# Performance work log

Measured on AMD Instinct MI355X. Metric: run time of the kernel, lower is better.

Reference implementation:

```python
import jax, jax.numpy as jnp
import numpy as np

D_MODEL = 2048
NUM_HEADS = 32
NUM_KV_GROUPS = 8
D_K = D_MODEL // NUM_HEADS  # 64
KV_DIM = D_K * NUM_KV_GROUPS  # 512
B, S = 2, 2048


def setup_inputs() -> dict:
    key = jax.random.key(0)
    ks = jax.random.split(key, 9)
    sd = 1.0 / np.sqrt(D_MODEL).astype(np.float32)
    return {
        "x": jax.random.normal(ks[0], (B, S, D_MODEL), jnp.float32),
        "wq": jax.random.normal(ks[1], (D_MODEL, D_MODEL), jnp.float32) * sd,
        "bq": jnp.zeros((D_MODEL,), jnp.float32),
        "wk": jax.random.normal(ks[2], (D_MODEL, KV_DIM), jnp.float32) * sd,
        "bk": jnp.zeros((KV_DIM,), jnp.float32),
        "wv": jax.random.normal(ks[3], (D_MODEL, KV_DIM), jnp.float32) * sd,
        "bv": jnp.zeros((KV_DIM,), jnp.float32),
        "wo": jax.random.normal(ks[4], (D_MODEL, D_MODEL), jnp.float32) * sd,
        "bo": jnp.zeros((D_MODEL,), jnp.float32),
    }


def reference(x, wq, bq, wk, bk, wv, bv, wo, bo):
    b, s, _ = x.shape
    # projections (torch Linear = x @ W^T + b; weights here stored as (in,out))
    Q = (x @ wq + bq).reshape(b, s, NUM_HEADS, D_K).transpose(0, 2, 1, 3)       # [B,H,S,dk]
    K = (x @ wk + bk).reshape(b, s, NUM_KV_GROUPS, D_K).transpose(0, 2, 1, 3)   # [B,G,S,dk]
    V = (x @ wv + bv).reshape(b, s, NUM_KV_GROUPS, D_K).transpose(0, 2, 1, 3)   # [B,G,S,dk]
    kv_repeat = NUM_HEADS // NUM_KV_GROUPS
    K_rep = jnp.repeat(K, kv_repeat, axis=1)  # [B,H,S,dk]
    V_rep = jnp.repeat(V, kv_repeat, axis=1)  # [B,H,S,dk]
    scale = 1.0 / jnp.sqrt(jnp.asarray(D_K, x.dtype))
    attn_scores = jnp.einsum("bhqd,bhkd->bhqk", Q, K_rep) * scale
    attn_weights = jax.nn.softmax(attn_scores, axis=-1)                          # [B,H,S,S]
    context = jnp.einsum("bhqk,bhkd->bhqd", attn_weights, V_rep)
    context = context.transpose(0, 2, 1, 3).reshape(b, s, D_MODEL)
    return context @ wo + bo
```

## Files before the change

kernel.cpp:

```cpp
#include <hip/hip_runtime.h>
#include <hip/hip_bf16.h>

typedef __bf16 v8bf16 __attribute__((ext_vector_type(8)));
typedef __bf16 bf16x4 __attribute__((ext_vector_type(4)));
typedef float  f32x4  __attribute__((ext_vector_type(4)));

#define D_MODEL 2048
#define S_LEN   2048
#define NHEADS  32
#define NGROUPS 8
#define DK      64
#define NTOK    4096
#define NQKV    3072
#define QSCALE  0.18033688011112042f

__device__ __forceinline__ void lds_load16(const void* g, void* l) {
  __builtin_amdgcn_global_load_lds(
      (__attribute__((address_space(1))) unsigned int*)g,
      (__attribute__((address_space(3))) unsigned int*)l, 16, 0, 0);
}

__global__ __launch_bounds__(256)
void cvt_f32_bf16(const float* __restrict__ in, __bf16* __restrict__ out, int n) {
  int i = (blockIdx.x * 256 + threadIdx.x) * 4;
  if (i >= n) return;
  float4 v = *(const float4*)(in + i);
  bf16x4 o = { (__bf16)v.x, (__bf16)v.y, (__bf16)v.z, (__bf16)v.w };
  *(bf16x4*)(out + i) = o;
}

__global__ __launch_bounds__(256)
void transpose_cvt(const float* __restrict__ in, __bf16* __restrict__ out, int R, int C) {
  __shared__ float tile[32][33];
  int tx = threadIdx.x, ty = threadIdx.y;
  int c0 = blockIdx.x * 32, r0 = blockIdx.y * 32;
#pragma unroll
  for (int j = 0; j < 4; j++)
    tile[ty + 8 * j][tx] = in[(size_t)(r0 + ty + 8 * j) * C + c0 + tx];
  __syncthreads();
#pragma unroll
  for (int j = 0; j < 4; j++)
    out[(size_t)(c0 + ty + 8 * j) * R + r0 + tx] = (__bf16)tile[tx][ty + 8 * j];
}

__global__ __launch_bounds__(256)
void transpose_bf16(const __bf16* __restrict__ in, __bf16* __restrict__ out,
                    int R, int C, int ldin, int ldout) {
  __shared__ __bf16 tile[32][33];
  int tx = threadIdx.x, ty = threadIdx.y;
  int c0 = blockIdx.x * 32, r0 = blockIdx.y * 32;
#pragma unroll
  for (int j = 0; j < 4; j++)
    tile[ty + 8 * j][tx] = in[(size_t)(r0 + ty + 8 * j) * ldin + c0 + tx];
  __syncthreads();
#pragma unroll
  for (int j = 0; j < 4; j++)
    out[(size_t)(c0 + ty + 8 * j) * ldout + r0 + tx] = tile[tx][ty + 8 * j];
}

template <int MODE>
__global__ __launch_bounds__(256, 2)
void gemm_bt(const __bf16* __restrict__ A, const __bf16* __restrict__ BT,
             const float* __restrict__ b0, const float* __restrict__ b1,
             const float* __restrict__ b2,
             __bf16* __restrict__ Cb, float* __restrict__ Cf,
             int M, int N, int K) {
  __shared__ __bf16 As[128 * 32];
  __shared__ __bf16 Bs[128 * 32];
  const int t = threadIdx.x;
  const int lane = t & 63, w = t >> 6;
  const int lr = lane & 15, lg = lane >> 4;
  const int gx = gridDim.x;
  const int flat = blockIdx.y * gx + blockIdx.x;
  const int cpx = (gx * gridDim.y) >> 3;
  const int sb = (flat & 7) * cpx + (flat >> 3);
  const int m0 = (sb / gx) * 128, n0 = (sb % gx) * 128;
  const int rm = (w >> 1) * 64, cn = (w & 1) * 64;
  const int srow = t >> 2, scol = (t & 3) * 8;

  const f32x4 fz = {0.f, 0.f, 0.f, 0.f};
  f32x4 acc[4][4];
#pragma unroll
  for (int mi = 0; mi < 4; mi++)
#pragma unroll
    for (int ni = 0; ni < 4; ni++) acc[mi][ni] = fz;

  for (int kt = 0; kt < K; kt += 32) {
    __syncthreads();
    lds_load16(A + (size_t)(m0 + srow) * K + kt + scol, As + w * 512);
    lds_load16(A + (size_t)(m0 + 64 + srow) * K + kt + scol, As + 2048 + w * 512);
    lds_load16(BT + (size_t)(n0 + srow) * K + kt + scol, Bs + w * 512);
    lds_load16(BT + (size_t)(n0 + 64 + srow) * K + kt + scol, Bs + 2048 + w * 512);
    __syncthreads();
    v8bf16 af[4], bfr[4];
#pragma unroll
    for (int i = 0; i < 4; i++)
      af[i] = *(const v8bf16*)&As[(rm + i * 16 + lr) * 32 + lg * 8];
#pragma unroll
    for (int i = 0; i < 4; i++)
      bfr[i] = *(const v8bf16*)&Bs[(cn + i * 16 + lr) * 32 + lg * 8];
#pragma unroll
    for (int mi = 0; mi < 4; mi++)
#pragma unroll
      for (int ni = 0; ni < 4; ni++)
        acc[mi][ni] = __builtin_amdgcn_mfma_f32_16x16x32_bf16(af[mi], bfr[ni], acc[mi][ni], 0, 0, 0);
  }

#pragma unroll
  for (int ni = 0; ni < 4; ni++) {
    int col = n0 + cn + ni * 16 + lr;
    float bias, scale = 1.0f;
    if (MODE == 0) {
      if (col < 2048)      { bias = b0[col];        scale = QSCALE; }
      else if (col < 2560) { bias = b1[col - 2048]; }
      else                 { bias = b2[col - 2560]; }
    } else {
      bias = b0[col];
    }
#pragma unroll
    for (int mi = 0; mi < 4; mi++)
#pragma unroll
      for (int r = 0; r < 4; r++) {
        int row = m0 + rm + mi * 16 + lg * 4 + r;
        float v = acc[mi][ni][r] + bias;
        if (MODE == 0) Cb[(size_t)row * N + col] = (__bf16)(v * scale);
        else           Cf[(size_t)row * N + col] = v;
      }
  }
}

__global__ __launch_bounds__(256, 4)
void attn_kernel(const __bf16* __restrict__ QKV, const __bf16* __restrict__ VT,
                 __bf16* __restrict__ ctx) {
  __shared__ __bf16 smem[18944];
  const int t = threadIdx.x;
  const int lane = t & 63, w = t >> 6;
  const int lr = lane & 15, lg = lane >> 4;
  const int flat = blockIdx.y * 16 + blockIdx.x;
  const int swz = (flat & 7) * 128 + (flat >> 3);
  const int qt = swz & 15, bh = swz >> 4;
  const int b = bh >> 5, h = bh & 31, g = h >> 2;
  const int q0 = qt * 128;
  const int scol = (((t & 7) ^ ((t >> 3) & 7)) << 3);

  v8bf16 qa[2][2];
#pragma unroll
  for (int mi = 0; mi < 2; mi++)
#pragma unroll
    for (int dk2 = 0; dk2 < 2; dk2++)
      qa[mi][dk2] = *(const v8bf16*)(QKV +
          (size_t)(b * S_LEN + q0 + w * 32 + mi * 16 + lr) * NQKV + h * DK + dk2 * 32 + lg * 8);

  const __bf16* ksrc0 = QKV + (size_t)(b * S_LEN + (t >> 3)) * NQKV + D_MODEL + g * DK + scol;
  const __bf16* vsrc0 = VT + (size_t)(g * DK + (t >> 3)) * NTOK + b * S_LEN + scol;

  lds_load16(ksrc0, smem + w * 512);
  lds_load16(ksrc0 + (size_t)32 * NQKV, smem + 2048 + w * 512);
  lds_load16(vsrc0, smem + 4096 + w * 512);
  lds_load16(vsrc0 + (size_t)32 * NTOK, smem + 4096 + 2048 + w * 512);
  __syncthreads();

  const int kloff0 = lr * 64 + ((lg * 8) ^ ((lr & 7) << 3));
  const int kloff1 = lr * 64 + ((32 + lg * 8) ^ ((lr & 7) << 3));
  __bf16* Pw = smem + 16384 + w * 640;

  const __bf16 one1 = (__bf16)1.0f;
  const v8bf16 ones = { one1, one1, one1, one1, one1, one1, one1, one1 };
  const f32x4 fz = {0.f, 0.f, 0.f, 0.f};
  f32x4 o[2][4], o_sum[2];
  o_sum[0] = fz; o_sum[1] = fz;
#pragma unroll
  for (int mi = 0; mi < 2; mi++)
#pragma unroll
    for (int nd = 0; nd < 4; nd++) o[mi][nd] = fz;
  int cur = 0;

  for (int kt = 0; kt < 32; kt++) {
    if (kt < 31) {
      __bf16* nb = smem + (cur ^ 1) * 8192;
      const __bf16* kn = ksrc0 + (size_t)(kt + 1) * 64 * NQKV;
      const __bf16* vn = vsrc0 + (size_t)(kt + 1) * 64;
      lds_load16(kn, nb + w * 512);
      lds_load16(kn + (size_t)32 * NQKV, nb + 2048 + w * 512);
      lds_load16(vn, nb + 4096 + w * 512);
      lds_load16(vn + (size_t)32 * NTOK, nb + 4096 + 2048 + w * 512);
    }
    const __bf16* Kb = smem + cur * 8192;
    const __bf16* k0 = Kb + kloff0;
    const __bf16* k1 = Kb + kloff1;

    f32x4 st[4][2];
#pragma unroll
    for (int ni = 0; ni < 4; ni++) { st[ni][0] = fz; st[ni][1] = fz; }
    __builtin_amdgcn_s_setprio(1);
#pragma unroll
    for (int ni = 0; ni < 4; ni++) {
      v8bf16 kb = *(const v8bf16*)(k0 + ni * 1024);
      st[ni][0] = __builtin_amdgcn_mfma_f32_16x16x32_bf16(kb, qa[0][0], st[ni][0], 0, 0, 0);
      st[ni][1] = __builtin_amdgcn_mfma_f32_16x16x32_bf16(kb, qa[1][0], st[ni][1], 0, 0, 0);
    }
#pragma unroll
    for (int ni = 0; ni < 4; ni++) {
      v8bf16 kb = *(const v8bf16*)(k1 + ni * 1024);
      st[ni][0] = __builtin_amdgcn_mfma_f32_16x16x32_bf16(kb, qa[0][1], st[ni][0], 0, 0, 0);
      st[ni][1] = __builtin_amdgcn_mfma_f32_16x16x32_bf16(kb, qa[1][1], st[ni][1], 0, 0, 0);
    }
    __builtin_amdgcn_s_setprio(0);

#pragma unroll
    for (int ks = 0; ks < 2; ks++) {
      const __bf16* vbase = (ks ? k1 : k0) + 4096;
#pragma unroll
      for (int mi = 0; mi < 2; mi++) {
#pragma unroll
        for (int ni2 = 0; ni2 < 2; ni2++) {
          f32x4 sv = st[2 * ks + ni2][mi];
          bf16x4 pk = { (__bf16)exp2f(sv[0]), (__bf16)exp2f(sv[1]),
                        (__bf16)exp2f(sv[2]), (__bf16)exp2f(sv[3]) };
          *(bf16x4*)(Pw + lr * 40 + ni2 * 16 + lg * 4) = pk;
        }
        v8bf16 pa = *(const v8bf16*)(Pw + lr * 40 + lg * 8);
        __builtin_amdgcn_s_setprio(1);
#pragma unroll
        for (int nd = 0; nd < 4; nd++) {
          v8bf16 vb = *(const v8bf16*)(vbase + nd * 1024);
          o[mi][nd] = __builtin_amdgcn_mfma_f32_16x16x32_bf16(pa, vb, o[mi][nd], 0, 0, 0);
        }
        o_sum[mi] = __builtin_amdgcn_mfma_f32_16x16x32_bf16(pa, ones, o_sum[mi], 0, 0, 0);
        __builtin_amdgcn_s_setprio(0);
      }
    }

    __syncthreads();
    cur ^= 1;
  }

#pragma unroll
  for (int mi = 0; mi < 2; mi++)
#pragma unroll
    for (int r = 0; r < 4; r++) {
      float inv = 1.0f / o_sum[mi][r];
      int row = b * S_LEN + q0 + w * 32 + mi * 16 + lg * 4 + r;
#pragma unroll
      for (int nd = 0; nd < 4; nd++)
        ctx[(size_t)row * D_MODEL + h * DK + nd * 16 + lr] = (__bf16)(o[mi][nd][r] * inv);
    }
}

extern "C" void kernel_launch(void* const* d_in, const int* in_sizes, int n_in,
                              void* d_out, int out_size, void* d_ws, size_t ws_size,
                              hipStream_t stream) {
  (void)in_sizes; (void)n_in; (void)out_size; (void)ws_size;
  const float* x  = (const float*)d_in[0];
  const float* wq = (const float*)d_in[1];
  const float* bq = (const float*)d_in[2];
  const float* wk = (const float*)d_in[3];
  const float* bk = (const float*)d_in[4];
  const float* wv = (const float*)d_in[5];
  const float* bv = (const float*)d_in[6];
  const float* wo = (const float*)d_in[7];
  const float* bo = (const float*)d_in[8];

  char* ws = (char*)d_ws;
  __bf16* xb    = (__bf16*)(ws);
  __bf16* wqkvT = (__bf16*)(ws + 16777216);
  __bf16* woT   = (__bf16*)(ws + 29360128);
  __bf16* QKVb  = (__bf16*)(ws + 37748736);
  __bf16* VbT   = (__bf16*)(ws + 62914560);
  __bf16* ctx   = (__bf16*)(ws + 67108864);

  dim3 tb(32, 8);
  cvt_f32_bf16<<<8192, 256, 0, stream>>>(x, xb, NTOK * D_MODEL);
  transpose_cvt<<<dim3(64, 64), tb, 0, stream>>>(wq, wqkvT, 2048, 2048);
  transpose_cvt<<<dim3(16, 64), tb, 0, stream>>>(wk, wqkvT + 2048 * 2048, 2048, 512);
  transpose_cvt<<<dim3(16, 64), tb, 0, stream>>>(wv, wqkvT + 2560 * 2048, 2048, 512);
  transpose_cvt<<<dim3(64, 64), tb, 0, stream>>>(wo, woT, 2048, 2048);

  gemm_bt<0><<<dim3(24, 32), 256, 0, stream>>>(xb, wqkvT, bq, bk, bv,
                                               QKVb, nullptr, NTOK, NQKV, 2048);
  transpose_bf16<<<dim3(16, 128), tb, 0, stream>>>(QKVb + 2560, VbT, 4096, 512, 3072, 4096);
  attn_kernel<<<dim3(16, 64), 256, 0, stream>>>(QKVb, VbT, ctx);
  gemm_bt<1><<<dim3(16, 32), 256, 0, stream>>>(ctx, woT, bo, nullptr, nullptr,
                                               nullptr, (float*)d_out, NTOK, 2048, 2048);
}
```

Baseline: 242.0 us.

## Double attention block to 8 waves over 256 queries sharing each K/V tile

The attention kernel now runs 512 threads per block covering 256 query rows instead of 128. Each K/V tile loaded into LDS is therefore reused by twice as many waves, which halves global K/V traffic and the number of blocks. The loop is also unrolled by two, and the P·V stage now writes both 16-row P fragments before issuing interleaved MFMAs for the two row groups. In exchange, fewer blocks are in flight, the larger LDS footprint lowers occupancy, and a block-wide barrier now spans 8 waves.

```diff
diff --git a/kernel.cpp b/kernel.cpp
--- a/kernel.cpp
+++ b/kernel.cpp
@@ -129,18 +129,18 @@
   }
 }
 
-__global__ __launch_bounds__(256, 4)
+__global__ __launch_bounds__(512, 2)
 void attn_kernel(const __bf16* __restrict__ QKV, const __bf16* __restrict__ VT,
                  __bf16* __restrict__ ctx) {
-  __shared__ __bf16 smem[18944];
+  __shared__ __bf16 smem[26624];
   const int t = threadIdx.x;
   const int lane = t & 63, w = t >> 6;
   const int lr = lane & 15, lg = lane >> 4;
-  const int flat = blockIdx.y * 16 + blockIdx.x;
-  const int swz = (flat & 7) * 128 + (flat >> 3);
-  const int qt = swz & 15, bh = swz >> 4;
+  const int flat = blockIdx.y * 8 + blockIdx.x;
+  const int swz = (flat & 7) * 64 + (flat >> 3);
+  const int qt = swz & 7, bh = swz >> 3;
   const int b = bh >> 5, h = bh & 31, g = h >> 2;
-  const int q0 = qt * 128;
+  const int q0 = qt * 256;
   const int scol = (((t & 7) ^ ((t >> 3) & 7)) << 3);
 
   v8bf16 qa[2][2];
@@ -151,18 +151,16 @@
       qa[mi][dk2] = *(const v8bf16*)(QKV +
           (size_t)(b * S_LEN + q0 + w * 32 + mi * 16 + lr) * NQKV + h * DK + dk2 * 32 + lg * 8);
 
-  const __bf16* ksrc0 = QKV + (size_t)(b * S_LEN + (t >> 3)) * NQKV + D_MODEL + g * DK + scol;
-  const __bf16* vsrc0 = VT + (size_t)(g * DK + (t >> 3)) * NTOK + b * S_LEN + scol;
-
-  lds_load16(ksrc0, smem + w * 512);
-  lds_load16(ksrc0 + (size_t)32 * NQKV, smem + 2048 + w * 512);
-  lds_load16(vsrc0, smem + 4096 + w * 512);
-  lds_load16(vsrc0 + (size_t)32 * NTOK, smem + 4096 + 2048 + w * 512);
+  const __bf16* kp = QKV + (size_t)(b * S_LEN + (t >> 3)) * NQKV + D_MODEL + g * DK + scol;
+  const __bf16* vp = VT + (size_t)(g * DK + (t >> 3)) * NTOK + b * S_LEN + scol;
+
+  lds_load16(kp, smem + t * 8);
+  lds_load16(vp, smem + 4096 + t * 8);
   __syncthreads();
 
   const int kloff0 = lr * 64 + ((lg * 8) ^ ((lr & 7) << 3));
   const int kloff1 = lr * 64 + ((32 + lg * 8) ^ ((lr & 7) << 3));
-  __bf16* Pw = smem + 16384 + w * 640;
+  __bf16* Pw = smem + 16384 + w * 1280;
 
   const __bf16 one1 = (__bf16)1.0f;
   const v8bf16 ones = { one1, one1, one1, one1, one1, one1, one1, one1 };
@@ -173,19 +171,17 @@
   for (int mi = 0; mi < 2; mi++)
 #pragma unroll
     for (int nd = 0; nd < 4; nd++) o[mi][nd] = fz;
-  int cur = 0;
-
+
+#pragma unroll 2
   for (int kt = 0; kt < 32; kt++) {
     if (kt < 31) {
-      __bf16* nb = smem + (cur ^ 1) * 8192;
-      const __bf16* kn = ksrc0 + (size_t)(kt + 1) * 64 * NQKV;
-      const __bf16* vn = vsrc0 + (size_t)(kt + 1) * 64;
-      lds_load16(kn, nb + w * 512);
-      lds_load16(kn + (size_t)32 * NQKV, nb + 2048 + w * 512);
-      lds_load16(vn, nb + 4096 + w * 512);
-      lds_load16(vn + (size_t)32 * NTOK, nb + 4096 + 2048 + w * 512);
-    }
-    const __bf16* Kb = smem + cur * 8192;
+      __bf16* nb = smem + ((kt & 1) ^ 1) * 8192;
+      lds_load16(kp + (size_t)64 * NQKV, nb + t * 8);
+      lds_load16(vp + 64, nb + 4096 + t * 8);
+      kp += (size_t)64 * NQKV;
+      vp += 64;
+    }
+    const __bf16* Kb = smem + (kt & 1) * 8192;
     const __bf16* k0 = Kb + kloff0;
     const __bf16* k1 = Kb + kloff1;
 
@@ -211,28 +207,29 @@
     for (int ks = 0; ks < 2; ks++) {
       const __bf16* vbase = (ks ? k1 : k0) + 4096;
 #pragma unroll
-      for (int mi = 0; mi < 2; mi++) {
+      for (int mi = 0; mi < 2; mi++)
 #pragma unroll
         for (int ni2 = 0; ni2 < 2; ni2++) {
           f32x4 sv = st[2 * ks + ni2][mi];
           bf16x4 pk = { (__bf16)exp2f(sv[0]), (__bf16)exp2f(sv[1]),
                         (__bf16)exp2f(sv[2]), (__bf16)exp2f(sv[3]) };
-          *(bf16x4*)(Pw + lr * 40 + ni2 * 16 + lg * 4) = pk;
+          *(bf16x4*)(Pw + (mi * 16 + lr) * 40 + ni2 * 16 + lg * 4) = pk;
         }
-        v8bf16 pa = *(const v8bf16*)(Pw + lr * 40 + lg * 8);
-        __builtin_amdgcn_s_setprio(1);
-#pragma unroll
-        for (int nd = 0; nd < 4; nd++) {
-          v8bf16 vb = *(const v8bf16*)(vbase + nd * 1024);
-          o[mi][nd] = __builtin_amdgcn_mfma_f32_16x16x32_bf16(pa, vb, o[mi][nd], 0, 0, 0);
-        }
-        o_sum[mi] = __builtin_amdgcn_mfma_f32_16x16x32_bf16(pa, ones, o_sum[mi], 0, 0, 0);
-        __builtin_amdgcn_s_setprio(0);
+      v8bf16 pa0 = *(const v8bf16*)(Pw + lr * 40 + lg * 8);
+      v8bf16 pa1 = *(const v8bf16*)(Pw + (16 + lr) * 40 + lg * 8);
+      __builtin_amdgcn_s_setprio(1);
+#pragma unroll
+      for (int nd = 0; nd < 4; nd++) {
+        v8bf16 vb = *(const v8bf16*)(vbase + nd * 1024);
+        o[0][nd] = __builtin_amdgcn_mfma_f32_16x16x32_bf16(pa0, vb, o[0][nd], 0, 0, 0);
+        o[1][nd] = __builtin_amdgcn_mfma_f32_16x16x32_bf16(pa1, vb, o[1][nd], 0, 0, 0);
       }
+      o_sum[0] = __builtin_amdgcn_mfma_f32_16x16x32_bf16(pa0, ones, o_sum[0], 0, 0, 0);
+      o_sum[1] = __builtin_amdgcn_mfma_f32_16x16x32_bf16(pa1, ones, o_sum[1], 0, 0, 0);
+      __builtin_amdgcn_s_setprio(0);
     }
 
     __syncthreads();
-    cur ^= 1;
   }
 
 #pragma unroll
@@ -279,7 +276,7 @@
   gemm_bt<0><<<dim3(24, 32), 256, 0, stream>>>(xb, wqkvT, bq, bk, bv,
                                                QKVb, nullptr, NTOK, NQKV, 2048);
   transpose_bf16<<<dim3(16, 128), tb, 0, stream>>>(QKVb + 2560, VbT, 4096, 512, 3072, 4096);
-  attn_kernel<<<dim3(16, 64), 256, 0, stream>>>(QKVb, VbT, ctx);
+  attn_kernel<<<dim3(8, 64), 512, 0, stream>>>(QKVb, VbT, ctx);
   gemm_bt<1><<<dim3(16, 32), 256, 0, stream>>>(ctx, woT, bo, nullptr, nullptr,
                                                nullptr, (float*)d_out, NTOK, 2048, 2048);
 }
```

Result: faster. 228.2 us (-5.7%).
